# Kernel tuning notes

Measured on AMD Instinct MI355X. Metric: run time of the kernel, lower is better.

The kernel has to match this reference:

```python
import jax, jax.numpy as jnp
import numpy as np

N, D, E = 50000, 128, 800000
BN_EPS = 1e-5


def _gcn(x, W, b, row, col, val):
    # dropout with p=0.0 is identity; h = x @ W; out = adj @ h + b (COO SpMM)
    h = x @ W                                    # [N, d]
    msg = val[:, None] * h[col]                  # [E, d] gather + scale
    agg = jax.ops.segment_sum(msg, row, num_segments=x.shape[0])  # scatter-add
    return agg + b


def _predictor(x, W1, b1, gamma, beta, a, W2, b2):
    h = x @ W1 + b1
    mu = jnp.mean(h, axis=0)
    var = jnp.mean((h - mu) ** 2, axis=0)        # biased var (torch BN train mode)
    hn = (h - mu) / jnp.sqrt(var + BN_EPS) * gamma + beta
    hp = jnp.where(hn >= 0, hn, a * hn)          # PReLU, single shared alpha
    return hp @ W2 + b2


def _byol_loss(p, t):
    pn = p / jnp.linalg.norm(p, axis=-1, keepdims=True)
    tn = t / jnp.linalg.norm(t, axis=-1, keepdims=True)
    return 2.0 - 2.0 * jnp.sum(pn * tn, axis=-1)


def setup_inputs() -> dict:
    key = jax.random.key(0)
    ks = jax.random.split(key, 16)
    xavier = float(np.sqrt(6.0 / (D + D)))
    x = jax.random.normal(ks[0], (N, D), dtype=jnp.float32)
    perb = 0.05 * jax.random.normal(ks[1], (N, D), dtype=jnp.float32)
    edge_row = jax.random.randint(ks[2], (E,), 0, N, dtype=jnp.int32)
    edge_col = jax.random.randint(ks[3], (E,), 0, N, dtype=jnp.int32)
    edge_val = jax.random.uniform(ks[4], (E,), dtype=jnp.float32)
    W = jax.random.uniform(ks[5], (D, D), minval=-xavier, maxval=xavier, dtype=jnp.float32)
    b = jnp.zeros((D,), dtype=jnp.float32)
    # target encoder is a deepcopy at init; give it its own values to test the math
    Wt = jax.random.uniform(ks[6], (D, D), minval=-xavier, maxval=xavier, dtype=jnp.float32)
    bt = jnp.zeros((D,), dtype=jnp.float32)
    lin = float(1.0 / np.sqrt(D))
    W1 = jax.random.uniform(ks[7], (D, D), minval=-lin, maxval=lin, dtype=jnp.float32)
    b1 = jax.random.uniform(ks[8], (D,), minval=-lin, maxval=lin, dtype=jnp.float32)
    bn_gamma = jnp.ones((D,), dtype=jnp.float32)
    bn_beta = jnp.zeros((D,), dtype=jnp.float32)
    prelu_a = jnp.asarray(0.25, dtype=jnp.float32)
    W2 = jax.random.uniform(ks[9], (D, D), minval=-lin, maxval=lin, dtype=jnp.float32)
    b2 = jax.random.uniform(ks[10], (D,), minval=-lin, maxval=lin, dtype=jnp.float32)
    return dict(x=x, perb=perb, edge_row=edge_row, edge_col=edge_col, edge_val=edge_val,
                W=W, b=b, Wt=Wt, bt=bt, W1=W1, b1=b1, bn_gamma=bn_gamma,
                bn_beta=bn_beta, prelu_a=prelu_a, W2=W2, b2=b2)


def reference(x, perb, edge_row, edge_col, edge_val, W, b, Wt, bt,
              W1, b1, bn_gamma, bn_beta, prelu_a, W2, b2):
    x1 = x
    x2 = x + perb
    enc_x2 = _gcn(x2, W, b, edge_row, edge_col, edge_val)
    embed = x2 + enc_x2
    online_x = _gcn(x1, W, b, edge_row, edge_col, edge_val)
    online_y = enc_x2
    target_y = jax.lax.stop_gradient(_gcn(x1, Wt, bt, edge_row, edge_col, edge_val))
    target_x = jax.lax.stop_gradient(_gcn(x2, Wt, bt, edge_row, edge_col, edge_val))
    px = _predictor(online_x, W1, b1, bn_gamma, bn_beta, prelu_a, W2, b2)
    py = _predictor(online_y, W1, b1, bn_gamma, bn_beta, prelu_a, W2, b2)
    loss = jnp.mean(_byol_loss(px, target_x) + _byol_loss(py, target_y))
    return embed, loss
```

## Files before the change

kernel.cpp:

```cpp
#include <hip/hip_runtime.h>
#include <stdint.h>

typedef unsigned short u16;
typedef unsigned int u32;
typedef __attribute__((ext_vector_type(8))) short bf16x8;
typedef __attribute__((ext_vector_type(4))) short bf16x4;
typedef __attribute__((ext_vector_type(4))) float f32x4;

#define DD 128
#define CAP 64
#define STRA 136
#define STRC1 264
#define STRCF 132

__device__ __forceinline__ float bflo(u32 u){ return __uint_as_float(u<<16); }
__device__ __forceinline__ float bfhi(u32 u){ return __uint_as_float(u & 0xffff0000u); }
__device__ __forceinline__ float bf2f(u16 u){ return __uint_as_float(((u32)u)<<16); }
__device__ __forceinline__ u16 f2bf(float f){
  u32 u = __float_as_uint(f);
  return (u16)((u + 0x7fffu + ((u>>16)&1u)) >> 16);
}

#define FMA8(g, vv) do { \
    acc[0] += (vv)*bflo((g).x); acc[1] += (vv)*bfhi((g).x); \
    acc[2] += (vv)*bflo((g).y); acc[3] += (vv)*bfhi((g).y); \
    acc[4] += (vv)*bflo((g).z); acc[5] += (vv)*bfhi((g).z); \
    acc[6] += (vv)*bflo((g).w); acc[7] += (vv)*bfhi((g).w); } while(0)

__global__ __launch_bounds__(256) void kU_init(
    const float* __restrict__ x, const float* __restrict__ perb,
    const float* __restrict__ W, const float* __restrict__ Wt,
    const float* __restrict__ W1, const float* __restrict__ W2,
    u16* __restrict__ T, u16* __restrict__ Bswz,
    u16* __restrict__ W1swz, u16* __restrict__ W2swz,
    int* __restrict__ deg, float* __restrict__ stats,
    float* __restrict__ gbuf, int N)
{
  int f = blockIdx.x*256 + threadIdx.x;
  if (f < N) deg[f] = 0;
  if (f < 512) stats[f] = 0.f;
  if (f < 64) gbuf[f] = 0.f;
  if (f < 65536) {
    int idx = f;
    if (idx < 32768) {
      int j = idx & 7, lane = (idx>>3)&63, nt = (idx>>9)&15, kt = idx>>13;
      int k = kt*32 + (lane>>4)*8 + j, n = nt*16 + (lane&15);
      float v = (n < DD) ? W[k*DD + n] : Wt[k*DD + (n-DD)];
      Bswz[idx] = f2bf(v);
    } else {
      int t = idx - 32768;
      int which = t >> 14; t &= 16383;
      int j = t & 7, lane = (t>>3)&63, nt = (t>>9)&7, kt = (t>>12)&3;
      int k = kt*32 + (lane>>4)*8 + j, n = nt*16 + (lane&15);
      const float* __restrict__ src = which ? W2 : W1;
      u16* __restrict__ dst = which ? W2swz : W1swz;
      dst[t] = f2bf(src[k*DD + n]);
    }
  }
  if (f < N*32) {
    int r = f >> 5, c8 = f & 31;
    const float* src = (c8 < 16) ? (x + (size_t)r*DD + c8*8)
                                 : (perb + (size_t)r*DD + (c8-16)*8);
    float4 a = *(const float4*)src;
    float4 bq = *(const float4*)(src + 4);
    bf16x8 o;
    o[0]=(short)f2bf(a.x); o[1]=(short)f2bf(a.y); o[2]=(short)f2bf(a.z); o[3]=(short)f2bf(a.w);
    o[4]=(short)f2bf(bq.x); o[5]=(short)f2bf(bq.y); o[6]=(short)f2bf(bq.z); o[7]=(short)f2bf(bq.w);
    *(bf16x8*)(T + (size_t)r*256 + c8*8) = o;
  }
}

__global__ __launch_bounds__(256) void k2_bucket(
    const int* __restrict__ row, const int* __restrict__ col,
    const float* __restrict__ val, int E, int* __restrict__ deg,
    int2* __restrict__ perm, int* __restrict__ ovfc, int* __restrict__ ovf)
{
  int e = blockIdx.x*256 + threadIdx.x;
  if (e >= E) return;
  int r = row[e];
  int slot = atomicAdd(&deg[r], 1);
  if (slot < CAP) {
    int2 cv; cv.x = col[e]; cv.y = __float_as_int(val[e]);
    perm[(size_t)r*CAP + slot] = cv;
  }
  else { int oi = atomicAdd(ovfc, 1); if (oi < 4096) ovf[oi] = e; }
}

__global__ __launch_bounds__(256) void k3_spmm(
    const int2* __restrict__ perm, const int* __restrict__ deg,
    const u16* __restrict__ T, u16* __restrict__ T2, int N)
{
  int row = blockIdx.x*4 + (threadIdx.x >> 6);
  int l = threadIdx.x & 63;
  if (row >= N) return;
  int dg = deg[row];
  dg = dg < 0 ? 0 : (dg > CAP ? CAP : dg);
  const int half = l >> 5, hl = l & 31;
  const int eoff = hl * 8;
  float acc[8] = {0.f,0.f,0.f,0.f,0.f,0.f,0.f,0.f};
  for (int base = 0; base < dg; base += 64) {
    int2 ev = make_int2(0, 0);
    if (base + l < dg) ev = perm[(size_t)row*CAP + base + l];
    int c = ev.x; float v = __int_as_float(ev.y);
    c = ((unsigned)c < (unsigned)N) ? c : 0;
    int mm = dg - base; if (mm > 64) mm = 64;
    int kmax = (mm + 1) & ~1;
    int j = 0;
    for (; j + 8 <= kmax; j += 8) {
      int i0 = j + half, i1 = j + 2 + half, i2 = j + 4 + half, i3 = j + 6 + half;
      int   c0 = __shfl(c, i0), c1 = __shfl(c, i1);
      int   c2 = __shfl(c, i2), c3 = __shfl(c, i3);
      float v0 = __shfl(v, i0), v1 = __shfl(v, i1);
      float v2 = __shfl(v, i2), v3 = __shfl(v, i3);
      uint4 g0 = *(const uint4*)(T + (size_t)c0*256 + eoff);
      uint4 g1 = *(const uint4*)(T + (size_t)c1*256 + eoff);
      uint4 g2 = *(const uint4*)(T + (size_t)c2*256 + eoff);
      uint4 g3 = *(const uint4*)(T + (size_t)c3*256 + eoff);
      FMA8(g0, v0); FMA8(g1, v1); FMA8(g2, v2); FMA8(g3, v3);
    }
    for (; j < kmax; j += 2) {
      int i0 = j + half;
      int   c0 = __shfl(c, i0);
      float v0 = __shfl(v, i0);
      uint4 g0 = *(const uint4*)(T + (size_t)c0*256 + eoff);
      FMA8(g0, v0);
    }
  }
  #pragma unroll
  for (int i = 0; i < 8; ++i) acc[i] += __shfl_xor(acc[i], 32);
  int sel = (hl >= 16) ? (hl - 16) : hl;
  bf16x8 ob;
  #pragma unroll
  for (int i = 0; i < 8; ++i) {
    float xv = __shfl(acc[i], sel);
    float o = (hl < 16) ? acc[i] : (xv + acc[i]);
    ob[i] = (short)f2bf(o);
  }
  if (half == 0)
    *(bf16x8*)(T2 + (size_t)row*256 + hl*8) = ob;
}

__global__ __launch_bounds__(256) void k3b_ovf(
    const int* __restrict__ rowI, const int* __restrict__ colI,
    const float* __restrict__ val, const int* __restrict__ ovfc,
    const int* __restrict__ ovf, const u16* __restrict__ T,
    u16* __restrict__ T2)
{
  int n = *ovfc; if (n > 4096) n = 4096;
  for (int i = 0; i < n; ++i) {
    int e = ovf[i];
    int r = rowI[e], c = colI[e];
    float v = val[e];
    int d = threadIdx.x;
    int dl = d & 127;
    float add = v * bf2f(T[(size_t)c*256 + dl]);
    if (d >= 128) add += v * bf2f(T[(size_t)c*256 + 128 + dl]);
    u16* p = &T2[(size_t)r*256 + d];
    *p = f2bf(bf2f(*p) + add);
  }
}

__global__ __launch_bounds__(256) void k4_gemm(
    const u16* __restrict__ T2, const u16* __restrict__ Bswz,
    const float* __restrict__ b, const float* __restrict__ bt,
    const u16* __restrict__ T,
    u16* __restrict__ AGGb, float* __restrict__ outE, int N)
{
  __shared__ __align__(16) u16 As[64*STRA];
  __shared__ __align__(16) u16 Cs[64*STRC1];
  const int tid = threadIdx.x;
  const int r0 = blockIdx.x * 32;
  #pragma unroll
  for (int i = 0; i < 4; ++i) {
    int f = tid + 256*i;
    int row = f >> 4, c8 = f & 15;
    int r = r0 + (row & 31);
    bf16x8 ch = {0,0,0,0,0,0,0,0};
    if (r < N) ch = *(const bf16x8*)(T2 + (size_t)r*256 + (row>>5)*128 + c8*8);
    *(bf16x8*)&As[row*STRA + c8*8] = ch;
  }
  __syncthreads();
  const int w = tid >> 6, l = tid & 63;
  const int m = l & 15, q = l >> 4;
  f32x4 acc[16];
  #pragma unroll
  for (int nt = 0; nt < 16; ++nt) acc[nt] = (f32x4){0.f,0.f,0.f,0.f};
  const int arow = w*16 + m;
  #pragma unroll
  for (int kt = 0; kt < 4; ++kt) {
    bf16x8 af = *(const bf16x8*)&As[arow*STRA + kt*32 + q*8];
    #pragma unroll
    for (int nt = 0; nt < 16; ++nt) {
      bf16x8 bf = *(const bf16x8*)(Bswz + ((size_t)(kt*16+nt)*64 + l)*8);
      acc[nt] = __builtin_amdgcn_mfma_f32_16x16x32_bf16(af, bf, acc[nt], 0, 0, 0);
    }
  }
  #pragma unroll
  for (int nt = 0; nt < 16; ++nt) {
    int n = nt*16 + m;
    float bv = (n < 128) ? b[n] : bt[n-128];
    #pragma unroll
    for (int i = 0; i < 4; ++i)
      Cs[(w*16 + q*4 + i)*STRC1 + nt*16 + m] = f2bf(acc[nt][i] + bv);
  }
  __syncthreads();
  {
    const int ar = tid >> 2, p = tid & 3;
    const int src = r0 + (ar & 31);
    if (src < N) {
      size_t grow = (size_t)src*2 + (ar >> 5);
      const u16* sp = &Cs[ar*STRC1 + p*64];
      u16* dp = AGGb + grow*256 + p*64;
      #pragma unroll
      for (int i = 0; i < 8; ++i)
        *(bf16x8*)(dp + i*8) = *(const bf16x8*)(sp + i*8);
    }
  }
  #pragma unroll
  for (int i = 0; i < 2; ++i) {
    int f = tid + 256*i;
    int rr = f >> 4, c8 = f & 15;
    int src = r0 + rr;
    if (src < N) {
      const u16* cp = &Cs[(32+rr)*STRC1 + c8*8];
      bf16x8 xv = *(const bf16x8*)(T + (size_t)src*256 + c8*8);
      bf16x8 pv = *(const bf16x8*)(T + (size_t)src*256 + 128 + c8*8);
      bf16x8 cv = *(const bf16x8*)cp;
      float4 e0, e1;
      e0.x = bf2f((u16)xv[0])+bf2f((u16)pv[0])+bf2f((u16)cv[0]);
      e0.y = bf2f((u16)xv[1])+bf2f((u16)pv[1])+bf2f((u16)cv[1]);
      e0.z = bf2f((u16)xv[2])+bf2f((u16)pv[2])+bf2f((u16)cv[2]);
      e0.w = bf2f((u16)xv[3])+bf2f((u16)pv[3])+bf2f((u16)cv[3]);
      e1.x = bf2f((u16)xv[4])+bf2f((u16)pv[4])+bf2f((u16)cv[4]);
      e1.y = bf2f((u16)xv[5])+bf2f((u16)pv[5])+bf2f((u16)cv[5]);
      e1.z = bf2f((u16)xv[6])+bf2f((u16)pv[6])+bf2f((u16)cv[6]);
      e1.w = bf2f((u16)xv[7])+bf2f((u16)pv[7])+bf2f((u16)cv[7]);
      float* er = outE + (size_t)src*DD + c8*8;
      *(float4*)er = e0;
      *(float4*)(er+4) = e1;
    }
  }
}

__global__ __launch_bounds__(256) void k5_gemm(
    const u16* __restrict__ AGGb, const u16* __restrict__ W1swz,
    const float* __restrict__ b1, u16* __restrict__ Px, u16* __restrict__ Py,
    float* __restrict__ partial, int N)
{
  __shared__ __align__(16) float Cs[64*STRCF];
  u16* As = (u16*)Cs;
  const int tid = threadIdx.x;
  const int seg = blockIdx.y;
  const int soff = seg ? 256 : 0;
  const int r0 = blockIdx.x * 64;
  #pragma unroll
  for (int i = 0; i < 4; ++i) {
    int f = tid + 256*i;
    int row = f >> 4, c8 = f & 15;
    int r = r0 + row;
    bf16x8 ch = {0,0,0,0,0,0,0,0};
    if (r < N) ch = *(const bf16x8*)(AGGb + (size_t)r*512 + soff + c8*8);
    *(bf16x8*)&As[row*STRA + c8*8] = ch;
  }
  __syncthreads();
  const int w = tid >> 6, l = tid & 63;
  const int m = l & 15, q = l >> 4;
  f32x4 acc[8];
  #pragma unroll
  for (int nt = 0; nt < 8; ++nt) acc[nt] = (f32x4){0.f,0.f,0.f,0.f};
  const int arow = w*16 + m;
  #pragma unroll
  for (int kt = 0; kt < 4; ++kt) {
    bf16x8 af = *(const bf16x8*)&As[arow*STRA + kt*32 + q*8];
    #pragma unroll
    for (int nt = 0; nt < 8; ++nt) {
      bf16x8 bf = *(const bf16x8*)(W1swz + ((size_t)(kt*8+nt)*64 + l)*8);
      acc[nt] = __builtin_amdgcn_mfma_f32_16x16x32_bf16(af, bf, acc[nt], 0, 0, 0);
    }
  }
  __syncthreads();
  const int rbase = r0 + w*16 + q*4;
  float* red = Cs;
  #pragma unroll
  for (int nt = 0; nt < 8; ++nt) {
    float bv = b1[nt*16 + m];
    float sum = 0.f, sq = 0.f;
    #pragma unroll
    for (int i = 0; i < 4; ++i) {
      if (rbase + i < N) acc[nt][i] += bv; else acc[nt][i] = 0.f;
      sum += acc[nt][i]; sq += acc[nt][i]*acc[nt][i];
    }
    sum += __shfl_xor(sum, 16); sum += __shfl_xor(sum, 32);
    sq  += __shfl_xor(sq, 16);  sq  += __shfl_xor(sq, 32);
    if (l < 16) {
      red[      w*128 + nt*16 + l] = sum;
      red[512 + w*128 + nt*16 + l] = sq;
    }
  }
  __syncthreads();
  {
    int type = tid >> 7, col = tid & 127;
    float v = red[type*512 + col] + red[type*512 + 128 + col]
            + red[type*512 + 256 + col] + red[type*512 + 384 + col];
    partial[((size_t)seg*gridDim.x + blockIdx.x)*256 + tid] = v;
  }
  __syncthreads();
  #pragma unroll
  for (int nt = 0; nt < 8; ++nt)
    #pragma unroll
    for (int i = 0; i < 4; ++i)
      Cs[(w*16 + q*4 + i)*STRCF + nt*16 + m] = acc[nt][i];
  __syncthreads();
  const int ar = tid >> 2, p = tid & 3;
  const int r = r0 + ar;
  u16* __restrict__ P = seg ? Py : Px;
  if (r < N) {
    const float* sp = &Cs[ar*STRCF + p*32];
    u16* dp = P + (size_t)r*DD + p*32;
    #pragma unroll
    for (int i = 0; i < 4; ++i) {
      bf16x8 ob;
      #pragma unroll
      for (int t2 = 0; t2 < 8; ++t2) ob[t2] = (short)f2bf(sp[i*8+t2]);
      *(bf16x8*)(dp + i*8) = ob;
    }
  }
}

__global__ __launch_bounds__(256) void k5b_stats(
    const float* __restrict__ partial, float* __restrict__ stats, int nb)
{
  int seg = blockIdx.y, chunk = blockIdx.x, t = threadIdx.x;
  int per = (nb + gridDim.x - 1) / gridDim.x;
  int lo = chunk*per, hi = lo+per; if (hi > nb) hi = nb;
  float s = 0.f;
  const float* p = partial + (size_t)seg*nb*256;
  for (int i = lo; i < hi; ++i) s += p[(size_t)i*256 + t];
  atomicAdd(&stats[seg*256 + t], s);
}

__global__ __launch_bounds__(256) void k6_gemm_loss(
    const u16* __restrict__ Px, const u16* __restrict__ Py,
    const u16* __restrict__ AGGb, const float* __restrict__ stats,
    const float* __restrict__ gamma, const float* __restrict__ beta,
    const float* __restrict__ aP, const u16* __restrict__ W2swz,
    const float* __restrict__ b2, float* __restrict__ gloss, int N)
{
  __shared__ __align__(16) float Cs[64*STRCF];
  u16* As = (u16*)Cs;
  __shared__ float s1s[128], s2s[128];
  __shared__ float gred[4];
  const int tid = threadIdx.x;
  const int seg = blockIdx.y;
  const u16* __restrict__ P = seg ? Py : Px;
  const int toff = seg ? 128 : 384;
  const float invN = 1.f / (float)N;
  if (tid < 128) {
    float mu = stats[seg*256 + tid] * invN;
    float var = stats[seg*256 + 128 + tid] * invN - mu*mu;
    float rstd = rsqrtf(var + 1e-5f);
    float s1 = rstd * gamma[tid];
    s1s[tid] = s1;
    s2s[tid] = beta[tid] - mu*s1;
  }
  const float alpha = aP[0];
  const int r0 = blockIdx.x * 64;
  __syncthreads();
  #pragma unroll
  for (int i = 0; i < 4; ++i) {
    int f = tid + 256*i;
    int row = f >> 4, c8 = f & 15;
    int r = r0 + row;
    bf16x8 ch = {0,0,0,0,0,0,0,0};
    if (r < N) ch = *(const bf16x8*)(P + (size_t)r*DD + c8*8);
    bf16x8 a;
    #pragma unroll
    for (int t2 = 0; t2 < 8; ++t2) {
      int colc = c8*8 + t2;
      float hv = bf2f((u16)ch[t2]);
      float hn = hv*s1s[colc] + s2s[colc];
      hn = hn >= 0.f ? hn : alpha*hn;
      a[t2] = (short)f2bf(hn);
    }
    *(bf16x8*)&As[row*STRA + c8*8] = a;
  }
  __syncthreads();
  const int w = tid >> 6, l = tid & 63;
  const int m = l & 15, q = l >> 4;
  f32x4 acc[8];
  #pragma unroll
  for (int nt = 0; nt < 8; ++nt) acc[nt] = (f32x4){0.f,0.f,0.f,0.f};
  const int arow = w*16 + m;
  #pragma unroll
  for (int kt = 0; kt < 4; ++kt) {
    bf16x8 af = *(const bf16x8*)&As[arow*STRA + kt*32 + q*8];
    #pragma unroll
    for (int nt = 0; nt < 8; ++nt) {
      bf16x8 bf = *(const bf16x8*)(W2swz + ((size_t)(kt*8+nt)*64 + l)*8);
      acc[nt] = __builtin_amdgcn_mfma_f32_16x16x32_bf16(af, bf, acc[nt], 0, 0, 0);
    }
  }
  __syncthreads();
  #pragma unroll
  for (int nt = 0; nt < 8; ++nt) {
    float bv = b2[nt*16 + m];
    #pragma unroll
    for (int i = 0; i < 4; ++i)
      Cs[(w*16 + q*4 + i)*STRCF + nt*16 + m] = acc[nt][i] + bv;
  }
  __syncthreads();
  {
    const int rt = tid >> 2, qq = tid & 3;
    const int r = r0 + rt;
    float pp = 0.f, tt = 0.f, pt = 0.f;
    if (r < N) {
      const float* prow = &Cs[rt*STRCF + qq*32];
      const u16* trow = AGGb + (size_t)r*512 + toff + qq*32;
      #pragma unroll
      for (int i = 0; i < 4; ++i) {
        float4 pa = *(const float4*)(prow + i*8);
        float4 pb = *(const float4*)(prow + i*8 + 4);
        uint4 twv = *(const uint4*)(trow + i*8);
        float t0=bflo(twv.x), t1=bfhi(twv.x), t2=bflo(twv.y), t3=bfhi(twv.y);
        float t4=bflo(twv.z), t5=bfhi(twv.z), t6=bflo(twv.w), t7=bfhi(twv.w);
        pp += pa.x*pa.x + pa.y*pa.y + pa.z*pa.z + pa.w*pa.w
            + pb.x*pb.x + pb.y*pb.y + pb.z*pb.z + pb.w*pb.w;
        tt += t0*t0 + t1*t1 + t2*t2 + t3*t3 + t4*t4 + t5*t5 + t6*t6 + t7*t7;
        pt += pa.x*t0 + pa.y*t1 + pa.z*t2 + pa.w*t3
            + pb.x*t4 + pb.y*t5 + pb.z*t6 + pb.w*t7;
      }
    }
    pp += __shfl_xor(pp, 1); pp += __shfl_xor(pp, 2);
    tt += __shfl_xor(tt, 1); tt += __shfl_xor(tt, 2);
    pt += __shfl_xor(pt, 1); pt += __shfl_xor(pt, 2);
    float lsum = (r < N) ? (2.f - 2.f * pt * rsqrtf(pp * tt)) : 0.f;
    lsum += __shfl_xor(lsum, 4);  lsum += __shfl_xor(lsum, 8);
    lsum += __shfl_xor(lsum, 16); lsum += __shfl_xor(lsum, 32);
    if (l == 0) gred[w] = lsum;
  }
  __syncthreads();
  if (tid == 0) atomicAdd(gloss, gred[0]+gred[1]+gred[2]+gred[3]);
}

__global__ void k7_loss(const float* __restrict__ gloss, float* __restrict__ out, int N, int total)
{
  out[total] = gloss[0] / (float)N;
}

extern "C" void kernel_launch(void* const* d_in, const int* in_sizes, int n_in,
                              void* d_out, int out_size, void* d_ws, size_t ws_size,
                              hipStream_t stream)
{
  const float* x    = (const float*)d_in[0];
  const float* perb = (const float*)d_in[1];
  const int*   erow = (const int*)d_in[2];
  const int*   ecol = (const int*)d_in[3];
  const float* eval_= (const float*)d_in[4];
  const float* W    = (const float*)d_in[5];
  const float* b    = (const float*)d_in[6];
  const float* Wt   = (const float*)d_in[7];
  const float* bt   = (const float*)d_in[8];
  const float* W1   = (const float*)d_in[9];
  const float* b1   = (const float*)d_in[10];
  const float* gam  = (const float*)d_in[11];
  const float* bet  = (const float*)d_in[12];
  const float* aP   = (const float*)d_in[13];
  const float* W2   = (const float*)d_in[14];
  const float* b2   = (const float*)d_in[15];
  const int N = in_sizes[0] / DD;
  const int E = in_sizes[2];
  const int NB5 = (N + 63)/64;

  char* ws = (char*)d_ws;
  size_t off = 0;
  auto alloc = [&](size_t bytes) -> void* {
    void* p = ws + off;
    off += (bytes + 255) & ~(size_t)255;
    return p;
  };
  u16*   AGGb = (u16*)  alloc((size_t)N*512*sizeof(u16));
  u16*   T    = (u16*)  alloc((size_t)N*256*sizeof(u16));
  u16*   T2   = (u16*)  alloc((size_t)N*256*sizeof(u16));
  int*   deg  = (int*)  alloc((size_t)N*sizeof(int));
  float* stats= (float*)alloc(512*sizeof(float));
  float* gloss= (float*)alloc(256);
  int*   ovfc = (int*)((char*)gloss + 64);
  int2*  perm = (int2*) alloc((size_t)N*CAP*sizeof(int2));
  int*   ovf  = (int*)  alloc(4096*sizeof(int));
  u16*   Bswz = (u16*)  alloc(32768*sizeof(u16));
  u16*   W1swz= (u16*)  alloc(16384*sizeof(u16));
  u16*   W2swz= (u16*)  alloc(16384*sizeof(u16));
  float* partial = (float*)alloc((size_t)2*NB5*256*sizeof(float));
  if (ws_size < off) return;

  u16* Px = T;
  u16* Py = Px + (size_t)N*DD;

  kU_init<<<(N*32 + 255)/256, 256, 0, stream>>>(x, perb, W, Wt, W1, W2,
                                                T, Bswz, W1swz, W2swz,
                                                deg, stats, gloss, N);
  k2_bucket<<<(E + 255)/256, 256, 0, stream>>>(erow, ecol, eval_, E, deg, perm, ovfc, ovf);
  k3_spmm<<<(N + 3)/4, 256, 0, stream>>>(perm, deg, T, T2, N);
  k3b_ovf<<<1, 256, 0, stream>>>(erow, ecol, eval_, ovfc, ovf, T, T2);
  k4_gemm<<<(N + 31)/32, 256, 0, stream>>>(T2, Bswz, b, bt, T, AGGb, (float*)d_out, N);
  k5_gemm<<<dim3(NB5, 2), 256, 0, stream>>>(AGGb, W1swz, b1, Px, Py, partial, N);
  k5b_stats<<<dim3(16, 2), 256, 0, stream>>>(partial, stats, NB5);
  k6_gemm_loss<<<dim3(NB5, 2), 256, 0, stream>>>(Px, Py, AGGb, stats, gam, bet, aP,
                                                 W2swz, b2, gloss, N);
  k7_loss<<<1, 1, 0, stream>>>(gloss, (float*)d_out, N, N*DD);
}
```

Before: 334.0 us.

## Fuse predictor first GEMM into encoder GEMM and pack edge entries to 32 bits

```diff
diff --git a/kernel.cpp b/kernel.cpp
--- a/kernel.cpp
+++ b/kernel.cpp
@@ -1,4 +1,5 @@
 #include <hip/hip_runtime.h>
+#include <hip/hip_fp16.h>
 #include <stdint.h>
 
 typedef unsigned short u16;
@@ -73,21 +74,22 @@
 __global__ __launch_bounds__(256) void k2_bucket(
     const int* __restrict__ row, const int* __restrict__ col,
     const float* __restrict__ val, int E, int* __restrict__ deg,
-    int2* __restrict__ perm, int* __restrict__ ovfc, int* __restrict__ ovf)
+    u32* __restrict__ perm, int* __restrict__ ovfc, int* __restrict__ ovf)
 {
   int e = blockIdx.x*256 + threadIdx.x;
   if (e >= E) return;
   int r = row[e];
   int slot = atomicAdd(&deg[r], 1);
   if (slot < CAP) {
-    int2 cv; cv.x = col[e]; cv.y = __float_as_int(val[e]);
-    perm[(size_t)r*CAP + slot] = cv;
+    u32 pk = (u32)(col[e] & 0xffff)
+           | ((u32)__half_as_ushort(__float2half(val[e])) << 16);
+    perm[(size_t)r*CAP + slot] = pk;
   }
   else { int oi = atomicAdd(ovfc, 1); if (oi < 4096) ovf[oi] = e; }
 }
 
 __global__ __launch_bounds__(256) void k3_spmm(
-    const int2* __restrict__ perm, const int* __restrict__ deg,
+    const u32* __restrict__ perm, const int* __restrict__ deg,
     const u16* __restrict__ T, u16* __restrict__ T2, int N)
 {
   int row = blockIdx.x*4 + (threadIdx.x >> 6);
@@ -99,19 +101,24 @@
   const int eoff = hl * 8;
   float acc[8] = {0.f,0.f,0.f,0.f,0.f,0.f,0.f,0.f};
   for (int base = 0; base < dg; base += 64) {
-    int2 ev = make_int2(0, 0);
-    if (base + l < dg) ev = perm[(size_t)row*CAP + base + l];
-    int c = ev.x; float v = __int_as_float(ev.y);
-    c = ((unsigned)c < (unsigned)N) ? c : 0;
+    u32 pk = 0;
+    if (base + l < dg) pk = perm[(size_t)row*CAP + base + l];
     int mm = dg - base; if (mm > 64) mm = 64;
     int kmax = (mm + 1) & ~1;
     int j = 0;
     for (; j + 8 <= kmax; j += 8) {
-      int i0 = j + half, i1 = j + 2 + half, i2 = j + 4 + half, i3 = j + 6 + half;
-      int   c0 = __shfl(c, i0), c1 = __shfl(c, i1);
-      int   c2 = __shfl(c, i2), c3 = __shfl(c, i3);
-      float v0 = __shfl(v, i0), v1 = __shfl(v, i1);
-      float v2 = __shfl(v, i2), v3 = __shfl(v, i3);
+      u32 p0 = (u32)__shfl((int)pk, j + half);
+      u32 p1 = (u32)__shfl((int)pk, j + 2 + half);
+      u32 p2 = (u32)__shfl((int)pk, j + 4 + half);
+      u32 p3 = (u32)__shfl((int)pk, j + 6 + half);
+      int c0 = p0 & 0xffff; c0 = (c0 < N) ? c0 : 0;
+      int c1 = p1 & 0xffff; c1 = (c1 < N) ? c1 : 0;
+      int c2 = p2 & 0xffff; c2 = (c2 < N) ? c2 : 0;
+      int c3 = p3 & 0xffff; c3 = (c3 < N) ? c3 : 0;
+      float v0 = __half2float(__ushort_as_half((u16)(p0 >> 16)));
+      float v1 = __half2float(__ushort_as_half((u16)(p1 >> 16)));
+      float v2 = __half2float(__ushort_as_half((u16)(p2 >> 16)));
+      float v3 = __half2float(__ushort_as_half((u16)(p3 >> 16)));
       uint4 g0 = *(const uint4*)(T + (size_t)c0*256 + eoff);
       uint4 g1 = *(const uint4*)(T + (size_t)c1*256 + eoff);
       uint4 g2 = *(const uint4*)(T + (size_t)c2*256 + eoff);
@@ -119,9 +126,9 @@
       FMA8(g0, v0); FMA8(g1, v1); FMA8(g2, v2); FMA8(g3, v3);
     }
     for (; j < kmax; j += 2) {
-      int i0 = j + half;
-      int   c0 = __shfl(c, i0);
-      float v0 = __shfl(v, i0);
+      u32 p0 = (u32)__shfl((int)pk, j + half);
+      int c0 = p0 & 0xffff; c0 = (c0 < N) ? c0 : 0;
+      float v0 = __half2float(__ushort_as_half((u16)(p0 >> 16)));
       uint4 g0 = *(const uint4*)(T + (size_t)c0*256 + eoff);
       FMA8(g0, v0);
     }
@@ -162,12 +169,16 @@
 
 __global__ __launch_bounds__(256) void k4_gemm(
     const u16* __restrict__ T2, const u16* __restrict__ Bswz,
+    const u16* __restrict__ W1swz,
     const float* __restrict__ b, const float* __restrict__ bt,
-    const u16* __restrict__ T,
-    u16* __restrict__ AGGb, float* __restrict__ outE, int N)
-{
-  __shared__ __align__(16) u16 As[64*STRA];
-  __shared__ __align__(16) u16 Cs[64*STRC1];
+    const float* __restrict__ b1, const u16* __restrict__ T,
+    u16* __restrict__ AGGb, float* __restrict__ outE,
+    u16* __restrict__ Px, u16* __restrict__ Py,
+    float* __restrict__ partial, int N, int NB)
+{
+  __shared__ __align__(16) u16 As1[64*STRA];
+  __shared__ __align__(16) float CsU[64*STRCF];
+  u16* Cs1 = (u16*)CsU;
   const int tid = threadIdx.x;
   const int r0 = blockIdx.x * 32;
   #pragma unroll
@@ -177,42 +188,43 @@
     int r = r0 + (row & 31);
     bf16x8 ch = {0,0,0,0,0,0,0,0};
     if (r < N) ch = *(const bf16x8*)(T2 + (size_t)r*256 + (row>>5)*128 + c8*8);
-    *(bf16x8*)&As[row*STRA + c8*8] = ch;
+    *(bf16x8*)&As1[row*STRA + c8*8] = ch;
   }
   __syncthreads();
   const int w = tid >> 6, l = tid & 63;
   const int m = l & 15, q = l >> 4;
-  f32x4 acc[16];
-  #pragma unroll
-  for (int nt = 0; nt < 16; ++nt) acc[nt] = (f32x4){0.f,0.f,0.f,0.f};
-  const int arow = w*16 + m;
-  #pragma unroll
-  for (int kt = 0; kt < 4; ++kt) {
-    bf16x8 af = *(const bf16x8*)&As[arow*STRA + kt*32 + q*8];
+  {
+    f32x4 acc[16];
+    #pragma unroll
+    for (int nt = 0; nt < 16; ++nt) acc[nt] = (f32x4){0.f,0.f,0.f,0.f};
+    const int arow = w*16 + m;
+    #pragma unroll
+    for (int kt = 0; kt < 4; ++kt) {
+      bf16x8 af = *(const bf16x8*)&As1[arow*STRA + kt*32 + q*8];
+      #pragma unroll
+      for (int nt = 0; nt < 16; ++nt) {
+        bf16x8 bfr = *(const bf16x8*)(Bswz + ((size_t)(kt*16+nt)*64 + l)*8);
+        acc[nt] = __builtin_amdgcn_mfma_f32_16x16x32_bf16(af, bfr, acc[nt], 0, 0, 0);
+      }
+    }
     #pragma unroll
     for (int nt = 0; nt < 16; ++nt) {
-      bf16x8 bf = *(const bf16x8*)(Bswz + ((size_t)(kt*16+nt)*64 + l)*8);
-      acc[nt] = __builtin_amdgcn_mfma_f32_16x16x32_bf16(af, bf, acc[nt], 0, 0, 0);
-    }
-  }
-  #pragma unroll
-  for (int nt = 0; nt < 16; ++nt) {
-    int n = nt*16 + m;
-    float bv = (n < 128) ? b[n] : bt[n-128];
-    #pragma unroll
-    for (int i = 0; i < 4; ++i)
-      Cs[(w*16 + q*4 + i)*STRC1 + nt*16 + m] = f2bf(acc[nt][i] + bv);
+      int n = nt*16 + m;
+      float bv = (n < 128) ? b[n] : bt[n-128];
+      #pragma unroll
+      for (int i = 0; i < 4; ++i)
+        Cs1[(w*16 + q*4 + i)*STRC1 + nt*16 + m] = f2bf(acc[nt][i] + bv);
+    }
   }
   __syncthreads();
   {
     const int ar = tid >> 2, p = tid & 3;
     const int src = r0 + (ar & 31);
     if (src < N) {
-      size_t grow = (size_t)src*2 + (ar >> 5);
-      const u16* sp = &Cs[ar*STRC1 + p*64];
-      u16* dp = AGGb + grow*256 + p*64;
+      u16* dp = AGGb + (size_t)src*256 + (ar>>5)*128 + p*32;
+      const u16* sp = &Cs1[ar*STRC1 + 128 + p*32];
       #pragma unroll
-      for (int i = 0; i < 8; ++i)
+      for (int i = 0; i < 4; ++i)
         *(bf16x8*)(dp + i*8) = *(const bf16x8*)(sp + i*8);
     }
   }
@@ -222,7 +234,7 @@
     int rr = f >> 4, c8 = f & 15;
     int src = r0 + rr;
     if (src < N) {
-      const u16* cp = &Cs[(32+rr)*STRC1 + c8*8];
+      const u16* cp = &Cs1[(32+rr)*STRC1 + c8*8];
       bf16x8 xv = *(const bf16x8*)(T + (size_t)src*256 + c8*8);
       bf16x8 pv = *(const bf16x8*)(T + (size_t)src*256 + 128 + c8*8);
       bf16x8 cv = *(const bf16x8*)cp;
@@ -240,55 +252,32 @@
       *(float4*)(er+4) = e1;
     }
   }
-}
-
-__global__ __launch_bounds__(256) void k5_gemm(
-    const u16* __restrict__ AGGb, const u16* __restrict__ W1swz,
-    const float* __restrict__ b1, u16* __restrict__ Px, u16* __restrict__ Py,
-    float* __restrict__ partial, int N)
-{
-  __shared__ __align__(16) float Cs[64*STRCF];
-  u16* As = (u16*)Cs;
-  const int tid = threadIdx.x;
-  const int seg = blockIdx.y;
-  const int soff = seg ? 256 : 0;
-  const int r0 = blockIdx.x * 64;
-  #pragma unroll
-  for (int i = 0; i < 4; ++i) {
-    int f = tid + 256*i;
-    int row = f >> 4, c8 = f & 15;
-    int r = r0 + row;
-    bf16x8 ch = {0,0,0,0,0,0,0,0};
-    if (r < N) ch = *(const bf16x8*)(AGGb + (size_t)r*512 + soff + c8*8);
-    *(bf16x8*)&As[row*STRA + c8*8] = ch;
-  }
-  __syncthreads();
-  const int w = tid >> 6, l = tid & 63;
-  const int m = l & 15, q = l >> 4;
-  f32x4 acc[8];
-  #pragma unroll
-  for (int nt = 0; nt < 8; ++nt) acc[nt] = (f32x4){0.f,0.f,0.f,0.f};
-  const int arow = w*16 + m;
-  #pragma unroll
-  for (int kt = 0; kt < 4; ++kt) {
-    bf16x8 af = *(const bf16x8*)&As[arow*STRA + kt*32 + q*8];
-    #pragma unroll
-    for (int nt = 0; nt < 8; ++nt) {
-      bf16x8 bf = *(const bf16x8*)(W1swz + ((size_t)(kt*8+nt)*64 + l)*8);
-      acc[nt] = __builtin_amdgcn_mfma_f32_16x16x32_bf16(af, bf, acc[nt], 0, 0, 0);
-    }
-  }
-  __syncthreads();
-  const int rbase = r0 + w*16 + q*4;
-  float* red = Cs;
+  f32x4 acc2[8];
+  #pragma unroll
+  for (int nt = 0; nt < 8; ++nt) acc2[nt] = (f32x4){0.f,0.f,0.f,0.f};
+  {
+    const int arow = w*16 + m;
+    #pragma unroll
+    for (int kt = 0; kt < 4; ++kt) {
+      bf16x8 af = *(const bf16x8*)&Cs1[arow*STRC1 + kt*32 + q*8];
+      #pragma unroll
+      for (int nt = 0; nt < 8; ++nt) {
+        bf16x8 bfr = *(const bf16x8*)(W1swz + ((size_t)(kt*8+nt)*64 + l)*8);
+        acc2[nt] = __builtin_amdgcn_mfma_f32_16x16x32_bf16(af, bfr, acc2[nt], 0, 0, 0);
+      }
+    }
+  }
+  __syncthreads();
+  float* red = CsU;
   #pragma unroll
   for (int nt = 0; nt < 8; ++nt) {
     float bv = b1[nt*16 + m];
     float sum = 0.f, sq = 0.f;
     #pragma unroll
     for (int i = 0; i < 4; ++i) {
-      if (rbase + i < N) acc[nt][i] += bv; else acc[nt][i] = 0.f;
-      sum += acc[nt][i]; sq += acc[nt][i]*acc[nt][i];
+      int src = r0 + ((w*16 + q*4 + i) & 31);
+      if (src < N) acc2[nt][i] += bv; else acc2[nt][i] = 0.f;
+      sum += acc2[nt][i]; sq += acc2[nt][i]*acc2[nt][i];
     }
     sum += __shfl_xor(sum, 16); sum += __shfl_xor(sum, 32);
     sq  += __shfl_xor(sq, 16);  sq  += __shfl_xor(sq, 32);
@@ -300,29 +289,31 @@
   __syncthreads();
   {
     int type = tid >> 7, col = tid & 127;
-    float v = red[type*512 + col] + red[type*512 + 128 + col]
-            + red[type*512 + 256 + col] + red[type*512 + 384 + col];
-    partial[((size_t)seg*gridDim.x + blockIdx.x)*256 + tid] = v;
+    float v0 = red[type*512 +   0 + col] + red[type*512 + 128 + col];
+    float v1 = red[type*512 + 256 + col] + red[type*512 + 384 + col];
+    partial[((size_t)0*NB + blockIdx.x)*256 + tid] = v0;
+    partial[((size_t)1*NB + blockIdx.x)*256 + tid] = v1;
   }
   __syncthreads();
   #pragma unroll
   for (int nt = 0; nt < 8; ++nt)
     #pragma unroll
     for (int i = 0; i < 4; ++i)
-      Cs[(w*16 + q*4 + i)*STRCF + nt*16 + m] = acc[nt][i];
-  __syncthreads();
-  const int ar = tid >> 2, p = tid & 3;
-  const int r = r0 + ar;
-  u16* __restrict__ P = seg ? Py : Px;
-  if (r < N) {
-    const float* sp = &Cs[ar*STRCF + p*32];
-    u16* dp = P + (size_t)r*DD + p*32;
-    #pragma unroll
-    for (int i = 0; i < 4; ++i) {
-      bf16x8 ob;
+      CsU[(w*16 + q*4 + i)*STRCF + nt*16 + m] = acc2[nt][i];
+  __syncthreads();
+  {
+    const int ar = tid >> 2, p = tid & 3;
+    const int src = r0 + (ar & 31);
+    if (src < N) {
+      const float* sp = &CsU[ar*STRCF + p*32];
+      u16* dp = ((ar >> 5) ? Py : Px) + (size_t)src*DD + p*32;
       #pragma unroll
-      for (int t2 = 0; t2 < 8; ++t2) ob[t2] = (short)f2bf(sp[i*8+t2]);
-      *(bf16x8*)(dp + i*8) = ob;
+      for (int i = 0; i < 4; ++i) {
+        bf16x8 ob;
+        #pragma unroll
+        for (int t2 = 0; t2 < 8; ++t2) ob[t2] = (short)f2bf(sp[i*8+t2]);
+        *(bf16x8*)(dp + i*8) = ob;
+      }
     }
   }
 }
@@ -353,7 +344,7 @@
   const int tid = threadIdx.x;
   const int seg = blockIdx.y;
   const u16* __restrict__ P = seg ? Py : Px;
-  const int toff = seg ? 128 : 384;
+  const int toff = seg ? 0 : 128;
   const float invN = 1.f / (float)N;
   if (tid < 128) {
     float mu = stats[seg*256 + tid] * invN;
@@ -396,8 +387,8 @@
     bf16x8 af = *(const bf16x8*)&As[arow*STRA + kt*32 + q*8];
     #pragma unroll
     for (int nt = 0; nt < 8; ++nt) {
-      bf16x8 bf = *(const bf16x8*)(W2swz + ((size_t)(kt*8+nt)*64 + l)*8);
-      acc[nt] = __builtin_amdgcn_mfma_f32_16x16x32_bf16(af, bf, acc[nt], 0, 0, 0);
+      bf16x8 bfr = *(const bf16x8*)(W2swz + ((size_t)(kt*8+nt)*64 + l)*8);
+      acc[nt] = __builtin_amdgcn_mfma_f32_16x16x32_bf16(af, bfr, acc[nt], 0, 0, 0);
     }
   }
   __syncthreads();
@@ -415,7 +406,7 @@
     float pp = 0.f, tt = 0.f, pt = 0.f;
     if (r < N) {
       const float* prow = &Cs[rt*STRCF + qq*32];
-      const u16* trow = AGGb + (size_t)r*512 + toff + qq*32;
+      const u16* trow = AGGb + (size_t)r*256 + toff + qq*32;
       #pragma unroll
       for (int i = 0; i < 4; ++i) {
         float4 pa = *(const float4*)(prow + i*8);
@@ -469,6 +460,7 @@
   const float* b2   = (const float*)d_in[15];
   const int N = in_sizes[0] / DD;
   const int E = in_sizes[2];
+  const int NB4 = (N + 31)/32;
   const int NB5 = (N + 63)/64;
 
   char* ws = (char*)d_ws;
@@ -478,23 +470,22 @@
     off += (bytes + 255) & ~(size_t)255;
     return p;
   };
-  u16*   AGGb = (u16*)  alloc((size_t)N*512*sizeof(u16));
+  u16*   AGGb = (u16*)  alloc((size_t)N*256*sizeof(u16));
   u16*   T    = (u16*)  alloc((size_t)N*256*sizeof(u16));
   u16*   T2   = (u16*)  alloc((size_t)N*256*sizeof(u16));
+  u16*   Px   = (u16*)  alloc((size_t)N*DD*sizeof(u16));
+  u16*   Py   = (u16*)  alloc((size_t)N*DD*sizeof(u16));
   int*   deg  = (int*)  alloc((size_t)N*sizeof(int));
   float* stats= (float*)alloc(512*sizeof(float));
   float* gloss= (float*)alloc(256);
   int*   ovfc = (int*)((char*)gloss + 64);
-  int2*  perm = (int2*) alloc((size_t)N*CAP*sizeof(int2));
+  u32*   perm = (u32*)  alloc((size_t)N*CAP*sizeof(u32));
   int*   ovf  = (int*)  alloc(4096*sizeof(int));
   u16*   Bswz = (u16*)  alloc(32768*sizeof(u16));
   u16*   W1swz= (u16*)  alloc(16384*sizeof(u16));
   u16*   W2swz= (u16*)  alloc(16384*sizeof(u16));
-  float* partial = (float*)alloc((size_t)2*NB5*256*sizeof(float));
+  float* partial = (float*)alloc((size_t)2*NB4*256*sizeof(float));
   if (ws_size < off) return;
-
-  u16* Px = T;
-  u16* Py = Px + (size_t)N*DD;
 
   kU_init<<<(N*32 + 255)/256, 256, 0, stream>>>(x, perb, W, Wt, W1, W2,
                                                 T, Bswz, W1swz, W2swz,
@@ -502,9 +493,9 @@
   k2_bucket<<<(E + 255)/256, 256, 0, stream>>>(erow, ecol, eval_, E, deg, perm, ovfc, ovf);
   k3_spmm<<<(N + 3)/4, 256, 0, stream>>>(perm, deg, T, T2, N);
   k3b_ovf<<<1, 256, 0, stream>>>(erow, ecol, eval_, ovfc, ovf, T, T2);
-  k4_gemm<<<(N + 31)/32, 256, 0, stream>>>(T2, Bswz, b, bt, T, AGGb, (float*)d_out, N);
-  k5_gemm<<<dim3(NB5, 2), 256, 0, stream>>>(AGGb, W1swz, b1, Px, Py, partial, N);
-  k5b_stats<<<dim3(16, 2), 256, 0, stream>>>(partial, stats, NB5);
+  k4_gemm<<<NB4, 256, 0, stream>>>(T2, Bswz, W1swz, b, bt, b1, T,
+                                   AGGb, (float*)d_out, Px, Py, partial, N, NB4);
+  k5b_stats<<<dim3(16, 2), 256, 0, stream>>>(partial, stats, NB4);
   k6_gemm_loss<<<dim3(NB5, 2), 256, 0, stream>>>(Px, Py, AGGb, stats, gam, bet, aP,
                                                  W2swz, b2, gloss, N);
   k7_loss<<<1, 1, 0, stream>>>(gloss, (float*)d_out, N, N*DD);
```

Result: no change. 332.1 us (-0.6%).
